# Kernel tuning notes

Hardware: AMD Instinct MI355X
Metric: run time of the kernel (lower is better)

## Reference

```python
import jax, jax.numpy as jnp
import numpy as np

N, K, C = 200000, 27, 64


def setup_inputs() -> dict:
    key = jax.random.key(0)
    k1, k2, k3, k4 = jax.random.split(key, 4)
    data = jax.random.normal(k1, (N, C), dtype=jnp.float32)
    # Xavier-like scale for depthwise weights (kdim, 1, C)
    weights = jax.random.normal(k2, (K, 1, C), dtype=jnp.float32) * 0.1
    neigh = jax.random.randint(k3, (N, K), 0, N, dtype=jnp.int32)
    invalid = jax.random.uniform(k4, (N, K)) < 0.05
    neigh = jnp.where(invalid, -1, neigh)
    return {"data": data, "weights": weights, "neigh": neigh}


def reference(data, weights, neigh):
    # buffer[i,k,c] = data[neigh[i,k], c] if neigh[i,k] >= 0 else 0
    valid = neigh >= 0                                   # [N, K]
    gathered = jnp.where(valid[:, :, None],
                         data[jnp.clip(neigh, 0)],       # [N, K, C]
                         jnp.zeros((), dtype=data.dtype))
    w = weights.reshape(K, C)                            # flatten(0,1)
    out = jnp.einsum('ikc,kc->ic', gathered, w)          # depthwise conv
    return out
```

## Files before the change

kernel.cpp:

```cpp
#include <hip/hip_runtime.h>
#include <stdint.h>


typedef float    v4f __attribute__((ext_vector_type(4)));
typedef uint32_t v2u __attribute__((ext_vector_type(2)));

constexpr int K   = 27;
constexpr int C   = 64;
constexpr int RPB = 32;

__global__ __launch_bounds__(256) void convert_kernel(
    const v4f* __restrict__ in,
    uint32_t*  __restrict__ outq,
    float*     __restrict__ scales,
    int nrows)
{
    const int l16 = threadIdx.x & 15;
    const int grp = threadIdx.x >> 4;
    const int r   = blockIdx.x * 16 + grp;
    if (r > nrows) return;
    if (r == nrows) {
        outq[r * 16 + l16] = 0u;
        if (l16 == 0) scales[r] = 0.f;
        return;
    }

    v4f a = __builtin_nontemporal_load(in + r * 16 + l16);
    float m = fmaxf(fmaxf(fabsf(a.x), fabsf(a.y)),
                    fmaxf(fabsf(a.z), fabsf(a.w)));
    m = fmaxf(m, __shfl_xor(m, 1));
    m = fmaxf(m, __shfl_xor(m, 2));
    m = fmaxf(m, __shfl_xor(m, 4));
    m = fmaxf(m, __shfl_xor(m, 8));

    const float inv = (m > 0.f) ? 127.f / m : 0.f;
    const int q0 = __float2int_rn(a.x * inv);
    const int q1 = __float2int_rn(a.y * inv);
    const int q2 = __float2int_rn(a.z * inv);
    const int q3 = __float2int_rn(a.w * inv);
    outq[r * 16 + l16] = (uint32_t)(q0 & 255)
                       | ((uint32_t)(q1 & 255) << 8)
                       | ((uint32_t)(q2 & 255) << 16)
                       | ((uint32_t)q3 << 24);
    if (l16 == 0) scales[r] = m * (1.f / 127.f);
}

__global__ __launch_bounds__(256) void gather_kernel(
    const v2u*   __restrict__ dataq,
    const float* __restrict__ scales,
    const float* __restrict__ weights,
    const int*   __restrict__ neigh,
    v4f*         __restrict__ out4,
    int nrows)
{
    __shared__ float w_lds[K * C];
    __shared__ int   n_lds[RPB * K];

    const int tid = threadIdx.x;
    for (int idx = tid; idx < K * C / 4; idx += 256)
        ((v4f*)w_lds)[idx] = ((const v4f*)weights)[idx];

    const long nbase = (long)blockIdx.x * RPB * K;
    const long ntot  = (long)nrows * K;
    for (int idx = tid; idx < RPB * K; idx += 256) {
        const long g = nbase + idx;
        n_lds[idx] = (g < ntot) ? __builtin_nontemporal_load(neigh + g) : -1;
    }
    __syncthreads();

    const int l     = tid & 7;
    const int group = tid >> 3;
    const int row   = blockIdx.x * RPB + group;
    if (row >= nrows) return;

    const int* __restrict__ nrow = n_lds + group * K;

    v2u   d[K];
    float s[K];
    #pragma unroll
    for (int j = 0; j < K; ++j) {
        const int n  = nrow[j];
        const int nz = (n < 0) ? nrows : n;
        d[j] = dataq[nz * 8 + l];
        s[j] = scales[nz];
    }

    v4f acc0 = (v4f){0.f, 0.f, 0.f, 0.f};
    v4f acc1 = (v4f){0.f, 0.f, 0.f, 0.f};
    #pragma unroll
    for (int j = 0; j < K; ++j) {
        const v4f* wv = (const v4f*)(w_lds + j * C + l * 8);
        const v4f ws0 = wv[0] * s[j];
        const v4f ws1 = wv[1] * s[j];
        const uint32_t lo = d[j].x, hi = d[j].y;
        acc0.x += (float)(int8_t)(lo      ) * ws0.x;
        acc0.y += (float)(int8_t)(lo >>  8) * ws0.y;
        acc0.z += (float)(int8_t)(lo >> 16) * ws0.z;
        acc0.w += (float)((int)lo >> 24)    * ws0.w;
        acc1.x += (float)(int8_t)(hi      ) * ws1.x;
        acc1.y += (float)(int8_t)(hi >>  8) * ws1.y;
        acc1.z += (float)(int8_t)(hi >> 16) * ws1.z;
        acc1.w += (float)((int)hi >> 24)    * ws1.w;
    }

    v4f* o = out4 + row * (C / 4) + l * 2;
    __builtin_nontemporal_store(acc0, o);
    __builtin_nontemporal_store(acc1, o + 1);
}

extern "C" void kernel_launch(void* const* d_in, const int* in_sizes, int n_in,
                              void* d_out, int out_size, void* d_ws, size_t ws_size,
                              hipStream_t stream) {
    const float* data    = (const float*)d_in[0];
    const float* weights = (const float*)d_in[1];
    const int*   neigh   = (const int*)d_in[2];
    v4f*         out4    = (v4f*)d_out;

    const int nrows = in_sizes[0] / C;
    uint32_t* dataq8 = (uint32_t*)d_ws;
    float*    scales = (float*)((char*)d_ws + (size_t)(nrows + 1) * 64);

    convert_kernel<<<(nrows + 1 + 15) / 16, 256, 0, stream>>>(
        (const v4f*)data, dataq8, scales, nrows);

    const int blocks = (nrows + RPB - 1) / RPB;
    gather_kernel<<<blocks, 256, 0, stream>>>(
        (const v2u*)dataq8, scales, weights, neigh, out4, nrows);
}
```

Measured before the change: 199.1 us.

## Bucket neighbor gathers by index range with grid-wide phase barriers

Switches to a persistent grid of 768 blocks, each handling 288 rows. Each row's 27 neighbor indices are sorted by the high bits of the index into 7 chunks, and all blocks walk the chunks in lockstep, separated by a spin-wait barrier on a global atomic counter. The goal is to keep the active slice of the quantized data table resident in cache during each phase and so cut random-gather misses. The cost is the per-row bucketing work, a spin barrier with a bounded timeout that assumes every block is resident at once, more LDS use, and extra memset and launch overhead.

```diff
diff --git a/kernel.cpp b/kernel.cpp
--- a/kernel.cpp
+++ b/kernel.cpp
@@ -5,9 +5,15 @@
 typedef float    v4f __attribute__((ext_vector_type(4)));
 typedef uint32_t v2u __attribute__((ext_vector_type(2)));
 
-constexpr int K   = 27;
-constexpr int C   = 64;
-constexpr int RPB = 32;
+constexpr int K      = 27;
+constexpr int C      = 64;
+constexpr int G      = 9;
+constexpr int GRID   = 768;
+constexpr int RPB    = G * 32;
+constexpr int NCHUNK = 7;
+constexpr int CSHIFT = 15;
+constexpr int SLOT   = 33;
+constexpr int SUB    = 32 * SLOT;
 
 __global__ __launch_bounds__(256) void convert_kernel(
     const v4f* __restrict__ in,
@@ -24,7 +30,6 @@
         if (l16 == 0) scales[r] = 0.f;
         return;
     }
-
     v4f a = __builtin_nontemporal_load(in + r * 16 + l16);
     float m = fmaxf(fmaxf(fabsf(a.x), fabsf(a.y)),
                     fmaxf(fabsf(a.z), fabsf(a.w)));
@@ -32,7 +37,6 @@
     m = fmaxf(m, __shfl_xor(m, 2));
     m = fmaxf(m, __shfl_xor(m, 4));
     m = fmaxf(m, __shfl_xor(m, 8));
-
     const float inv = (m > 0.f) ? 127.f / m : 0.f;
     const int q0 = __float2int_rn(a.x * inv);
     const int q1 = __float2int_rn(a.y * inv);
@@ -46,66 +50,148 @@
 }
 
 __global__ __launch_bounds__(256) void gather_kernel(
-    const v2u*   __restrict__ dataq,
+    const v2u*   __restrict__ dq,
     const float* __restrict__ scales,
     const float* __restrict__ weights,
     const int*   __restrict__ neigh,
     v4f*         __restrict__ out4,
+    unsigned*    __restrict__ ctr,
     int nrows)
 {
-    __shared__ float w_lds[K * C];
-    __shared__ int   n_lds[RPB * K];
-
-    const int tid = threadIdx.x;
+    __shared__ float    w_lds[K * C];
+    __shared__ uint32_t slab[G * SUB];
+
+    const int tid   = threadIdx.x;
+    const int l     = tid & 7;
+    const int group = tid >> 3;
+
     for (int idx = tid; idx < K * C / 4; idx += 256)
         ((v4f*)w_lds)[idx] = ((const v4f*)weights)[idx];
 
-    const long nbase = (long)blockIdx.x * RPB * K;
-    const long ntot  = (long)nrows * K;
-    for (int idx = tid; idx < RPB * K; idx += 256) {
-        const long g = nbase + idx;
-        n_lds[idx] = (g < ntot) ? __builtin_nontemporal_load(neigh + g) : -1;
+    const int  rowbase = blockIdx.x * RPB;
+    const long ntot    = (long)nrows * K;
+
+    for (int g = 0; g < G; ++g) {
+        const long base = (long)rowbase * K + (long)g * 32 * K;
+        for (int j = tid; j < 32 * K; j += 256) {
+            const long p = base + j;
+            const int  n = (p < ntot)
+                         ? __builtin_nontemporal_load(neigh + p) : -1;
+            slab[g * SUB + j] = (unsigned)(n < 0 ? nrows : n);
+        }
     }
     __syncthreads();
 
-    const int l     = tid & 7;
-    const int group = tid >> 3;
-    const int row   = blockIdx.x * RPB + group;
-    if (row >= nrows) return;
-
-    const int* __restrict__ nrow = n_lds + group * K;
-
-    v2u   d[K];
-    float s[K];
+    for (int g = 0; g < G; ++g) {
+        unsigned nn[K];
+        const int row = rowbase + g * 32 + group;
+        if (l == 0) {
+            #pragma unroll
+            for (int i = 0; i < K; ++i)
+                nn[i] = slab[g * SUB + group * K + i];
+        }
+        __syncthreads();
+        if (l == 0) {
+            uint64_t offp = 0;
+            if (row < nrows) {
+                uint64_t cntp = 0;
+                #pragma unroll
+                for (int i = 0; i < K; ++i)
+                    cntp += 1ull << ((nn[i] >> CSHIFT) * 8);
+                unsigned run = 0;
+                #pragma unroll
+                for (int cc = 1; cc < 8; ++cc) {
+                    run += (unsigned)((cntp >> (8 * (cc - 1))) & 255);
+                    offp |= (uint64_t)run << (8 * cc);
+                }
+                uint64_t posp = offp;
+                #pragma unroll
+                for (int i = 0; i < K; ++i) {
+                    const unsigned c   = nn[i] >> CSHIFT;
+                    const unsigned pos = (unsigned)((posp >> (8 * c)) & 255);
+                    slab[(g * 32 + group) * SLOT + pos] =
+                        (nn[i] << 5) | (unsigned)i;
+                    posp += 1ull << (8 * c);
+                }
+            }
+            slab[(g * 32 + group) * SLOT + 28] = (uint32_t)offp;
+            slab[(g * 32 + group) * SLOT + 29] = (uint32_t)(offp >> 32);
+        }
+    }
+    __syncthreads();
+
+    v4f a0[G], a1[G];
     #pragma unroll
-    for (int j = 0; j < K; ++j) {
-        const int n  = nrow[j];
-        const int nz = (n < 0) ? nrows : n;
-        d[j] = dataq[nz * 8 + l];
-        s[j] = scales[nz];
-    }
-
-    v4f acc0 = (v4f){0.f, 0.f, 0.f, 0.f};
-    v4f acc1 = (v4f){0.f, 0.f, 0.f, 0.f};
+    for (int g = 0; g < G; ++g) {
+        a0[g] = (v4f){0.f, 0.f, 0.f, 0.f};
+        a1[g] = (v4f){0.f, 0.f, 0.f, 0.f};
+    }
+    const unsigned padE = (unsigned)nrows << 5;
+
+    for (int c = 0; c < NCHUNK; ++c) {
+        #pragma unroll
+        for (int g = 0; g < G; ++g) {
+            const int rs = g * 32 + group;
+            const uint64_t offp = (uint64_t)slab[rs * SLOT + 28]
+                                | ((uint64_t)slab[rs * SLOT + 29] << 32);
+            const int lo = (int)((offp >> (8 * c)) & 255);
+            const int hi = (int)((offp >> (8 * c + 8)) & 255);
+            for (int j = lo; j < hi; j += 4) {
+                unsigned e[4]; v2u d[4]; float s[4];
+                #pragma unroll
+                for (int t = 0; t < 4; ++t) {
+                    const int idx = j + t;
+                    e[t] = (idx < hi) ? slab[rs * SLOT + idx] : padE;
+                }
+                #pragma unroll
+                for (int t = 0; t < 4; ++t) {
+                    const unsigned n = e[t] >> 5;
+                    d[t] = dq[n * 8 + l];
+                    s[t] = scales[n];
+                }
+                #pragma unroll
+                for (int t = 0; t < 4; ++t) {
+                    const unsigned k  = e[t] & 31;
+                    const v4f* wv = (const v4f*)(w_lds + k * C + l * 8);
+                    const v4f ws0 = wv[0] * s[t];
+                    const v4f ws1 = wv[1] * s[t];
+                    const uint32_t lov = d[t].x, hiv = d[t].y;
+                    a0[g].x += (float)(int8_t)(lov      ) * ws0.x;
+                    a0[g].y += (float)(int8_t)(lov >>  8) * ws0.y;
+                    a0[g].z += (float)(int8_t)(lov >> 16) * ws0.z;
+                    a0[g].w += (float)((int)lov >> 24)    * ws0.w;
+                    a1[g].x += (float)(int8_t)(hiv      ) * ws1.x;
+                    a1[g].y += (float)(int8_t)(hiv >>  8) * ws1.y;
+                    a1[g].z += (float)(int8_t)(hiv >> 16) * ws1.z;
+                    a1[g].w += (float)((int)hiv >> 24)    * ws1.w;
+                }
+            }
+        }
+        if (c + 1 < NCHUNK) {
+            __syncthreads();
+            if (tid == 0) {
+                atomicAdd(&ctr[c], 1u);
+                int it = 0;
+                while (__hip_atomic_load(&ctr[c], __ATOMIC_RELAXED,
+                                         __HIP_MEMORY_SCOPE_AGENT)
+                           < (unsigned)GRID && it < 8192) {
+                    __builtin_amdgcn_s_sleep(2);
+                    ++it;
+                }
+            }
+            __syncthreads();
+        }
+    }
+
     #pragma unroll
-    for (int j = 0; j < K; ++j) {
-        const v4f* wv = (const v4f*)(w_lds + j * C + l * 8);
-        const v4f ws0 = wv[0] * s[j];
-        const v4f ws1 = wv[1] * s[j];
-        const uint32_t lo = d[j].x, hi = d[j].y;
-        acc0.x += (float)(int8_t)(lo      ) * ws0.x;
-        acc0.y += (float)(int8_t)(lo >>  8) * ws0.y;
-        acc0.z += (float)(int8_t)(lo >> 16) * ws0.z;
-        acc0.w += (float)((int)lo >> 24)    * ws0.w;
-        acc1.x += (float)(int8_t)(hi      ) * ws1.x;
-        acc1.y += (float)(int8_t)(hi >>  8) * ws1.y;
-        acc1.z += (float)(int8_t)(hi >> 16) * ws1.z;
-        acc1.w += (float)((int)hi >> 24)    * ws1.w;
-    }
-
-    v4f* o = out4 + row * (C / 4) + l * 2;
-    __builtin_nontemporal_store(acc0, o);
-    __builtin_nontemporal_store(acc1, o + 1);
+    for (int g = 0; g < G; ++g) {
+        const int row = rowbase + g * 32 + group;
+        if (row < nrows) {
+            v4f* o = out4 + row * (C / 4) + l * 2;
+            __builtin_nontemporal_store(a0[g], o);
+            __builtin_nontemporal_store(a1[g], o + 1);
+        }
+    }
 }
 
 extern "C" void kernel_launch(void* const* d_in, const int* in_sizes, int n_in,
@@ -117,13 +203,19 @@
     v4f*         out4    = (v4f*)d_out;
 
     const int nrows = in_sizes[0] / C;
-    uint32_t* dataq8 = (uint32_t*)d_ws;
-    float*    scales = (float*)((char*)d_ws + (size_t)(nrows + 1) * 64);
+
+    uint32_t* dataq = (uint32_t*)d_ws;
+    const size_t dq_bytes = (size_t)(nrows + 1) * 64;
+    float* scales = (float*)((char*)d_ws + dq_bytes);
+    const size_t sc_bytes = (size_t)(nrows + 1) * 4;
+    unsigned* ctr = (unsigned*)((char*)d_ws +
+        ((dq_bytes + sc_bytes + 127) & ~(size_t)127));
 
     convert_kernel<<<(nrows + 1 + 15) / 16, 256, 0, stream>>>(
-        (const v4f*)data, dataq8, scales, nrows);
-
-    const int blocks = (nrows + RPB - 1) / RPB;
-    gather_kernel<<<blocks, 256, 0, stream>>>(
-        (const v2u*)dataq8, scales, weights, neigh, out4, nrows);
+        (const v4f*)data, dataq, scales, nrows);
+
+    hipMemsetAsync(ctr, 0, 64, stream);
+
+    gather_kernel<<<GRID, 256, 0, stream>>>(
+        (const v2u*)dataq, scales, weights, neigh, out4, ctr, nrows);
 }
```

Result: slower. 582.4 us (+192.5%).

## Sort per-row neighbor indices and process rows in persistent multi-row blocks

Applied to the files above, without the earlier changes.

Each block now handles 9 groups of 32 rows on a fixed grid of 695 blocks. For each row, the 27 neighbor indices, tagged with their tap index, are sorted in registers with a bitonic network. The int8 gathers are then issued in sorted order, in batches of 9, and the weight LDS rows are padded to a stride of 68. The aim is better cache locality for the random gathers and amortized neighbor/weight staging, at the cost of heavy per-thread ALU work for the sort, repeated redundantly by all 8 lanes of a row, and fewer loads in flight at once.

```diff
diff --git a/kernel.cpp b/kernel.cpp
--- a/kernel.cpp
+++ b/kernel.cpp
@@ -5,9 +5,12 @@
 typedef float    v4f __attribute__((ext_vector_type(4)));
 typedef uint32_t v2u __attribute__((ext_vector_type(2)));
 
-constexpr int K   = 27;
-constexpr int C   = 64;
-constexpr int RPB = 32;
+constexpr int K    = 27;
+constexpr int C    = 64;
+constexpr int G    = 9;
+constexpr int GRID = 695;
+constexpr int RPB  = G * 32;
+constexpr int WS   = 68;
 
 __global__ __launch_bounds__(256) void convert_kernel(
     const v4f* __restrict__ in,
@@ -24,7 +27,6 @@
         if (l16 == 0) scales[r] = 0.f;
         return;
     }
-
     v4f a = __builtin_nontemporal_load(in + r * 16 + l16);
     float m = fmaxf(fmaxf(fabsf(a.x), fabsf(a.y)),
                     fmaxf(fabsf(a.z), fabsf(a.w)));
@@ -32,7 +34,6 @@
     m = fmaxf(m, __shfl_xor(m, 2));
     m = fmaxf(m, __shfl_xor(m, 4));
     m = fmaxf(m, __shfl_xor(m, 8));
-
     const float inv = (m > 0.f) ? 127.f / m : 0.f;
     const int q0 = __float2int_rn(a.x * inv);
     const int q1 = __float2int_rn(a.y * inv);
@@ -46,66 +47,106 @@
 }
 
 __global__ __launch_bounds__(256) void gather_kernel(
-    const v2u*   __restrict__ dataq,
+    const v2u*   __restrict__ dq,
     const float* __restrict__ scales,
     const float* __restrict__ weights,
     const int*   __restrict__ neigh,
     v4f*         __restrict__ out4,
     int nrows)
 {
-    __shared__ float w_lds[K * C];
-    __shared__ int   n_lds[RPB * K];
+    __shared__ float    w_lds[K * WS];
+    __shared__ uint32_t n_lds[RPB * K];
 
-    const int tid = threadIdx.x;
-    for (int idx = tid; idx < K * C / 4; idx += 256)
-        ((v4f*)w_lds)[idx] = ((const v4f*)weights)[idx];
+    const int tid   = threadIdx.x;
+    const int l     = tid & 7;
+    const int group = tid >> 3;
 
-    const long nbase = (long)blockIdx.x * RPB * K;
-    const long ntot  = (long)nrows * K;
-    for (int idx = tid; idx < RPB * K; idx += 256) {
-        const long g = nbase + idx;
-        n_lds[idx] = (g < ntot) ? __builtin_nontemporal_load(neigh + g) : -1;
+    for (int idx = tid; idx < K * 16; idx += 256) {
+        const int k = idx >> 4, part = idx & 15;
+        ((v4f*)(w_lds + k * WS))[part] = ((const v4f*)weights)[idx];
+    }
+
+    const int  rowbase = blockIdx.x * RPB;
+    const long ntot    = (long)nrows * K;
+    const long base    = (long)rowbase * K;
+    for (int j = tid; j < RPB * K; j += 256) {
+        const long p = base + j;
+        const int  n = (p < ntot) ? __builtin_nontemporal_load(neigh + p)
+                                  : -1;
+        n_lds[j] = (unsigned)(n < 0 ? nrows : n);
     }
     __syncthreads();
 
-    const int l     = tid & 7;
-    const int group = tid >> 3;
-    const int row   = blockIdx.x * RPB + group;
-    if (row >= nrows) return;
+    #pragma unroll 1
+    for (int g = 0; g < G; ++g) {
+        const int rs  = g * 32 + group;
+        const int row = rowbase + rs;
 
-    const int* __restrict__ nrow = n_lds + group * K;
+        unsigned a[32];
+        #pragma unroll
+        for (int i = 0; i < K; ++i)
+            a[i] = (n_lds[rs * K + i] << 5) | (unsigned)i;
+        #pragma unroll
+        for (int i = K; i < 32; ++i) a[i] = 0xFFFFFFFFu;
 
-    v2u   d[K];
-    float s[K];
-    #pragma unroll
-    for (int j = 0; j < K; ++j) {
-        const int n  = nrow[j];
-        const int nz = (n < 0) ? nrows : n;
-        d[j] = dataq[nz * 8 + l];
-        s[j] = scales[nz];
+        #pragma unroll
+        for (int p = 1; p < 32; p <<= 1) {
+            #pragma unroll
+            for (int k = p; k >= 1; k >>= 1) {
+                #pragma unroll
+                for (int j = k & (p - 1); j + k < 32; j += 2 * k) {
+                    #pragma unroll
+                    for (int i = 0; i < k; ++i) {
+                        if (i + j + k < 32 &&
+                            (i + j) / (2 * p) == (i + j + k) / (2 * p)) {
+                            const unsigned x = a[i + j];
+                            const unsigned y = a[i + j + k];
+                            a[i + j]     = x < y ? x : y;
+                            a[i + j + k] = x < y ? y : x;
+                        }
+                    }
+                }
+            }
+        }
+
+        v4f acc0 = (v4f){0.f, 0.f, 0.f, 0.f};
+        v4f acc1 = (v4f){0.f, 0.f, 0.f, 0.f};
+
+        #pragma unroll
+        for (int b = 0; b < K; b += 9) {
+            unsigned e[9]; v2u d[9]; float s[9];
+            #pragma unroll
+            for (int j = 0; j < 9; ++j) e[j] = a[b + j];
+            #pragma unroll
+            for (int j = 0; j < 9; ++j) {
+                const unsigned n = e[j] >> 5;
+                d[j] = dq[n * 8 + l];
+                s[j] = scales[n];
+            }
+            #pragma unroll
+            for (int j = 0; j < 9; ++j) {
+                const unsigned k = e[j] & 31;
+                const v4f* wv = (const v4f*)(w_lds + k * WS + l * 8);
+                const v4f ws0 = wv[0] * s[j];
+                const v4f ws1 = wv[1] * s[j];
+                const uint32_t lov = d[j].x, hiv = d[j].y;
+                acc0.x += (float)(int8_t)(lov      ) * ws0.x;
+                acc0.y += (float)(int8_t)(lov >>  8) * ws0.y;
+                acc0.z += (float)(int8_t)(lov >> 16) * ws0.z;
+                acc0.w += (float)((int)lov >> 24)    * ws0.w;
+                acc1.x += (float)(int8_t)(hiv      ) * ws1.x;
+                acc1.y += (float)(int8_t)(hiv >>  8) * ws1.y;
+                acc1.z += (float)(int8_t)(hiv >> 16) * ws1.z;
+                acc1.w += (float)((int)hiv >> 24)    * ws1.w;
+            }
+        }
+
+        if (row < nrows) {
+            v4f* o = out4 + row * (C / 4) + l * 2;
+            __builtin_nontemporal_store(acc0, o);
+            __builtin_nontemporal_store(acc1, o + 1);
+        }
     }
-
-    v4f acc0 = (v4f){0.f, 0.f, 0.f, 0.f};
-    v4f acc1 = (v4f){0.f, 0.f, 0.f, 0.f};
-    #pragma unroll
-    for (int j = 0; j < K; ++j) {
-        const v4f* wv = (const v4f*)(w_lds + j * C + l * 8);
-        const v4f ws0 = wv[0] * s[j];
-        const v4f ws1 = wv[1] * s[j];
-        const uint32_t lo = d[j].x, hi = d[j].y;
-        acc0.x += (float)(int8_t)(lo      ) * ws0.x;
-        acc0.y += (float)(int8_t)(lo >>  8) * ws0.y;
-        acc0.z += (float)(int8_t)(lo >> 16) * ws0.z;
-        acc0.w += (float)((int)lo >> 24)    * ws0.w;
-        acc1.x += (float)(int8_t)(hi      ) * ws1.x;
-        acc1.y += (float)(int8_t)(hi >>  8) * ws1.y;
-        acc1.z += (float)(int8_t)(hi >> 16) * ws1.z;
-        acc1.w += (float)((int)hi >> 24)    * ws1.w;
-    }
-
-    v4f* o = out4 + row * (C / 4) + l * 2;
-    __builtin_nontemporal_store(acc0, o);
-    __builtin_nontemporal_store(acc1, o + 1);
 }
 
 extern "C" void kernel_launch(void* const* d_in, const int* in_sizes, int n_in,
@@ -117,13 +158,14 @@
     v4f*         out4    = (v4f*)d_out;
 
     const int nrows = in_sizes[0] / C;
-    uint32_t* dataq8 = (uint32_t*)d_ws;
-    float*    scales = (float*)((char*)d_ws + (size_t)(nrows + 1) * 64);
+
+    uint32_t* dataq = (uint32_t*)d_ws;
+    const size_t dq_bytes = (size_t)(nrows + 1) * 64;
+    float* scales = (float*)((char*)d_ws + dq_bytes);
 
     convert_kernel<<<(nrows + 1 + 15) / 16, 256, 0, stream>>>(
-        (const v4f*)data, dataq8, scales, nrows);
+        (const v4f*)data, dataq, scales, nrows);
 
-    const int blocks = (nrows + RPB - 1) / RPB;
-    gather_kernel<<<blocks, 256, 0, stream>>>(
-        (const v2u*)dataq8, scales, weights, neigh, out4, nrows);
+    gather_kernel<<<GRID, 256, 0, stream>>>(
+        (const v2u*)dataq, scales, weights, neigh, out4, nrows);
 }
```

Measured after the change: 296.3 us. +48.8%, slower.
